# Performance work log

Hardware: AMD Instinct MI355X
Metric: run time of the kernel (lower is better)

## Reference

```python
import jax, jax.numpy as jnp
import numpy as np

B, N, M, C = 4, 4096, 300, 1152
SA_H, SA_D = 36, 32           # linear self-attention heads / head dim
CA_H = 16                     # cross-attention heads
INNER_SA = SA_H * SA_D        # 1152
INNER_FF = int(C * 2.5)       # 2880
EPS = 1e-6


def _ln(x):
    # LayerNorm without affine, eps=1e-6
    mu = x.mean(-1, keepdims=True)
    var = x.var(-1, keepdims=True)
    return (x - mu) / jnp.sqrt(var + EPS)


def setup_inputs() -> dict:
    key = jax.random.key(0)
    ks = jax.random.split(key, 24)
    p = lambda i, shape: jax.random.normal(ks[i], shape, jnp.float32) * 0.02
    return {
        "x": jax.random.normal(ks[0], (B, N, C), jnp.float32),
        "conditioning": jax.random.normal(ks[1], (B, M, C), jnp.float32),
        "t_emb": jax.random.normal(ks[2], (B, C), jnp.float32),
        # linear self-attention (qkv has no bias)
        "w_qkv": p(3, (C, 3 * INNER_SA)),
        "w_sa_out": p(4, (INNER_SA, C)),
        "b_sa_out": jnp.zeros((C,), jnp.float32),
        # norm_cross (affine LayerNorm)
        "gamma_cross": jnp.ones((C,), jnp.float32),
        "beta_cross": jnp.zeros((C,), jnp.float32),
        # cross-attention
        "w_q": p(5, (C, C)), "b_q": jnp.zeros((C,), jnp.float32),
        "w_kv": p(6, (C, 2 * C)), "b_kv": jnp.zeros((2 * C,), jnp.float32),
        "w_co": p(7, (C, C)), "b_co": jnp.zeros((C,), jnp.float32),
        # MixFFN
        "w_fc1": p(8, (C, 2 * INNER_FF)), "b_fc1": jnp.zeros((2 * INNER_FF,), jnp.float32),
        "dw_kernel": p(9, (3, 3, 1, INNER_FF)),  # depthwise conv, HWIO
        "dw_bias": jnp.zeros((INNER_FF,), jnp.float32),
        "w_fc2": p(10, (INNER_FF, C)), "b_fc2": jnp.zeros((C,), jnp.float32),
        # adaLN modulation
        "w_ada": p(11, (C, 6 * C)), "b_ada": jnp.zeros((6 * C,), jnp.float32),
        "sst": jax.random.normal(ks[12], (6, C), jnp.float32) * 0.02,
    }


def reference(x, conditioning, t_emb, w_qkv, w_sa_out, b_sa_out,
              gamma_cross, beta_cross, w_q, b_q, w_kv, b_kv, w_co, b_co,
              w_fc1, b_fc1, dw_kernel, dw_bias, w_fc2, b_fc2,
              w_ada, b_ada, sst):
    Bx, Nx, Cx = x.shape
    ada = jax.nn.silu(t_emb) @ w_ada + b_ada          # (B, 6C)
    ada = sst[None] + ada.reshape(Bx, 6, Cx)          # (B, 6, C)
    shift_sa, scale_sa, gate_sa, shift_ff, scale_ff, gate_ff = (
        ada[:, 0], ada[:, 1], ada[:, 2], ada[:, 3], ada[:, 4], ada[:, 5])

    # --- modulated linear self-attention (ReLU kernel) ---
    xn = _ln(x) * (1.0 + scale_sa[:, None]) + shift_sa[:, None]
    qkv = (xn @ w_qkv).reshape(Bx, Nx, 3, SA_H, SA_D)
    q = jax.nn.relu(qkv[:, :, 0])
    k = jax.nn.relu(qkv[:, :, 1])
    v = qkv[:, :, 2]
    kv = jnp.einsum('bnhd,bnhe->bhde', k, v)                  # (B,H,D,D)
    out = jnp.einsum('bnhd,bhde->bnhe', q, kv)                # (B,N,H,D)
    denom = jnp.einsum('bnhd,bhd->bnh', q, k.sum(1)) + 1e-6   # (B,N,H)
    out = (out / denom[..., None]).reshape(Bx, Nx, INNER_SA)
    x = x + gate_sa[:, None] * (out @ w_sa_out + b_sa_out)

    # --- cross-attention (softmax) ---
    xc = _ln(x) * gamma_cross + beta_cross
    hd = Cx // CA_H
    qc = (xc @ w_q + b_q).reshape(Bx, Nx, CA_H, hd)
    kvc = (conditioning @ w_kv + b_kv).reshape(Bx, M, 2, CA_H, hd)
    kc, vc = kvc[:, :, 0], kvc[:, :, 1]
    attn = jnp.einsum('bnhd,bmhd->bhnm', qc, kc) * (hd ** -0.5)
    attn = jax.nn.softmax(attn, axis=-1)
    oc = jnp.einsum('bhnm,bmhd->bnhd', attn, vc).reshape(Bx, Nx, Cx)
    x = x + oc @ w_co + b_co

    # --- modulated GLU-dwconv FFN ---
    xn = _ln(x) * (1.0 + scale_ff[:, None]) + shift_ff[:, None]
    gv = xn @ w_fc1 + b_fc1
    gate, val = gv[..., :INNER_FF], gv[..., INNER_FF:]
    h = jax.nn.silu(gate) * val
    hw = int(round(Nx ** 0.5))
    h = h.reshape(Bx, hw, hw, INNER_FF)                       # NHWC
    h = jax.lax.conv_general_dilated(
        h, dw_kernel, window_strides=(1, 1), padding='SAME',
        dimension_numbers=('NHWC', 'HWIO', 'NHWC'),
        feature_group_count=INNER_FF) + dw_bias
    h = h.reshape(Bx, Nx, INNER_FF)
    x = x + gate_ff[:, None] * (h @ w_fc2 + b_fc2)
    return x
```

## Files before the change

kernel.cpp:

```cpp
#include <hip/hip_runtime.h>

typedef __bf16 bf16_t;
typedef __attribute__((ext_vector_type(8))) __bf16 bf16x8;
typedef __attribute__((ext_vector_type(4))) __bf16 bf16x4;
typedef __attribute__((ext_vector_type(4))) float f32x4;

#define DEVINL __device__ __forceinline__

DEVINL void gload16(const void* g, void* l) {
  __builtin_amdgcn_global_load_lds(
      (const __attribute__((address_space(1))) void*)g,
      (__attribute__((address_space(3))) void*)l, 16, 0, 0);
}

template <int OUT>
__global__ __launch_bounds__(512) void gemm256r(
    const bf16_t* __restrict__ A, const bf16_t* __restrict__ Bt,
    void* __restrict__ Cv, int M, int N, int K,
    const float* __restrict__ bias, const float* __restrict__ resid,
    const float* __restrict__ gate, int GM)
{
  __shared__ __align__(16) bf16_t sL[4][2][256 * 32];
  const int tid = threadIdx.x;
  const int lane = tid & 63;
  const int wave = tid >> 6;
  const int wr = wave >> 2;
  const int wc = wave & 3;

  const int nbx = gridDim.x, nby = gridDim.y;
  const int nwg = nbx * nby;
  int lin = (int)blockIdx.y * nbx + (int)blockIdx.x;
  {
    const int q = nwg >> 3, rr = nwg & 7;
    const int xcd = lin & 7, idx = lin >> 3;
    lin = (xcd < rr ? xcd * (q + 1) : rr * (q + 1) + (xcd - rr) * q) + idx;
  }
  const int per_grp = GM * nbx;
  const int gid = lin / per_grp;
  const int rem = lin - gid * per_grp;
  const int gsz = min(GM, nby - gid * GM);
  const long tileM = (long)(gid * GM + rem % gsz) * 256;
  const long tileN = (long)(rem / gsz) * 256;

  const int r0 = tid >> 2;
  const int c0 = (((tid & 3) - (r0 >> 2)) & 3) * 8;

  auto STAGE = [&](int slot, int kt) {
    const bf16_t* ga = A + (tileM + r0) * (long)K + kt + c0;
    const bf16_t* gb = Bt + (tileN + r0) * (long)K + kt + c0;
    char* la = (char*)&sL[slot][0][0] + tid * 16;
    char* lb = (char*)&sL[slot][1][0] + tid * 16;
    gload16(ga, la);
    gload16(ga + 128 * (long)K, la + 8192);
    gload16(gb, lb);
    gload16(gb + 128 * (long)K, lb + 8192);
  };

  f32x4 acc[8][4] = {};
  const int NT = K >> 5;

  STAGE(0, 0); STAGE(1, 32); STAGE(2, 64);
  asm volatile("s_waitcnt vmcnt(8)" ::: "memory");
  asm volatile("s_barrier" ::: "memory");

  const int r = lane & 15;
  const int kg = lane >> 4;
  const int sw = ((kg + (r >> 2)) & 3) * 16;
  const int abyte = (wr * 128 + r) * 64 + sw;
  const int bbyte = (wc * 64 + r) * 64 + sw;

  for (int t = 0; t < NT; ++t) {
    if (t + 3 < NT) STAGE((t + 3) & 3, (t + 3) << 5);
    const char* pA = (const char*)&sL[t & 3][0][0];
    const char* pB = (const char*)&sL[t & 3][1][0];
    bf16x8 a[8], b[4];
#pragma unroll
    for (int n = 0; n < 4; ++n) b[n] = *(const bf16x8*)(pB + bbyte + n * 1024);
#pragma unroll
    for (int m = 0; m < 8; ++m) a[m] = *(const bf16x8*)(pA + abyte + m * 1024);
    __builtin_amdgcn_s_setprio(1);
#pragma unroll
    for (int m = 0; m < 8; ++m)
#pragma unroll
      for (int n = 0; n < 4; ++n)
        acc[m][n] = __builtin_amdgcn_mfma_f32_16x16x32_bf16(a[m], b[n],
                                                            acc[m][n], 0, 0, 0);
    __builtin_amdgcn_s_setprio(0);
    if (t + 1 >= NT) break;
    if (t + 3 < NT)       asm volatile("s_waitcnt vmcnt(8)" ::: "memory");
    else if (t + 3 == NT) asm volatile("s_waitcnt vmcnt(4)" ::: "memory");
    else                  asm volatile("s_waitcnt vmcnt(0)" ::: "memory");
    asm volatile("s_barrier" ::: "memory");
  }

  const long row0 = tileM + wr * 128 + ((lane >> 4) * 4);
  const int col0 = (int)tileN + wc * 64 + r;
  if constexpr (OUT == 4) {
#pragma unroll
    for (int m = 0; m < 8; ++m) {
#pragma unroll
      for (int n = 0; n < 4; n += 2) {
        const int base = (int)tileN + wc * 64 + n * 16;
        if (base < 5760) {
          const int hcol = (base >> 1) + r;
          const float bg = bias[hcol];
          const float bv = bias[2880 + hcol];
#pragma unroll
          for (int j = 0; j < 4; ++j) {
            const long row = row0 + m * 16 + j;
            const float g = acc[m][n][j] + bg;
            const float v = acc[m][n + 1][j] + bv;
            const float sg = g / (1.0f + __expf(-g));
            ((bf16_t*)Cv)[row * 2880 + hcol] = (bf16_t)(sg * v);
          }
        }
      }
    }
    return;
  }
#pragma unroll
  for (int m = 0; m < 8; ++m) {
#pragma unroll
    for (int n = 0; n < 4; ++n) {
      const int col = col0 + n * 16;
      if (col < N) {
        const float bb = bias ? bias[col] : 0.0f;
#pragma unroll
        for (int j = 0; j < 4; ++j) {
          const long row = row0 + m * 16 + j;
          const long idx = row * (long)N + col;
          const float v = acc[m][n][j] + bb;
          if constexpr (OUT == 1) {
            const float g = gate ? gate[(row >> 12) * 6912 + col] : 1.0f;
            const float rv = resid ? resid[idx] : 0.0f;
            ((float*)Cv)[idx] = rv + g * v;
          } else {
            ((bf16_t*)Cv)[idx] = (bf16_t)v;
          }
        }
      }
    }
  }
}

template <int OUT>
__global__ __launch_bounds__(256) void gemm_bt(
    const bf16_t* __restrict__ A, const bf16_t* __restrict__ Bt,
    void* __restrict__ Cv, int M, int N, int K,
    long strideA, long strideB, long strideC,
    const float* __restrict__ bias, const float* __restrict__ resid,
    const float* __restrict__ gate, int GM)
{
  __shared__ __align__(16) bf16_t sA[128 * 32];
  __shared__ __align__(16) bf16_t sB[128 * 32];
  const int tid = threadIdx.x;
  const int lane = tid & 63;
  const int wave = tid >> 6;
  const bf16_t* Ab = A + (size_t)blockIdx.z * strideA;
  const bf16_t* Bb = Bt + (size_t)blockIdx.z * strideB;

  const int nbx = gridDim.x, nby = gridDim.y;
  const int nwg = nbx * nby;
  int lin = (int)blockIdx.y * nbx + (int)blockIdx.x;
  {
    const int q = nwg >> 3, rr = nwg & 7;
    const int xcd = lin & 7, idx = lin >> 3;
    lin = (xcd < rr ? xcd * (q + 1) : rr * (q + 1) + (xcd - rr) * q) + idx;
  }
  const int per_grp = GM * nbx;
  const int gid = lin / per_grp;
  const int rem = lin - gid * per_grp;
  const int gsz = min(GM, nby - gid * GM);
  const long tileM = (long)(gid * GM + rem % gsz) * 128;
  const long tileN = (long)(rem / gsz) * 128;
  const int wr = wave >> 1, wc = wave & 1;

  f32x4 acc[4][4] = {};

  const int srow = lane >> 2;
  const int skcol = (lane & 3) * 8;
  const bf16_t* gA0 = Ab + (tileM + wave * 16 + srow) * (long)K + skcol;
  const bf16_t* gB0 = Bb + (tileN + wave * 16 + srow) * (long)K + skcol;
  bf16_t* lA0 = sA + wave * 512;
  bf16_t* lB0 = sB + wave * 512;
  const long rs64 = 64L * K;

  const int aoff = (wr * 64 + (lane & 15)) * 32 + (lane >> 4) * 8;
  const int boff = (wc * 64 + (lane & 15)) * 32 + (lane >> 4) * 8;

  for (int kt = 0; kt < K; kt += 32) {
    __syncthreads();
    gload16(gA0 + kt, lA0);
    gload16(gA0 + kt + rs64, lA0 + 2048);
    gload16(gB0 + kt, lB0);
    gload16(gB0 + kt + rs64, lB0 + 2048);
    __syncthreads();
    bf16x8 av[4], bv[4];
#pragma unroll
    for (int m = 0; m < 4; ++m) av[m] = *(const bf16x8*)&sA[aoff + m * 512];
#pragma unroll
    for (int n = 0; n < 4; ++n) bv[n] = *(const bf16x8*)&sB[boff + n * 512];
#pragma unroll
    for (int m = 0; m < 4; ++m)
#pragma unroll
      for (int n = 0; n < 4; ++n)
        acc[m][n] = __builtin_amdgcn_mfma_f32_16x16x32_bf16(av[m], bv[n],
                                                            acc[m][n], 0, 0, 0);
  }

  const long row0 = tileM + wr * 64 + ((lane >> 4) * 4);
  const int col0 = (int)tileN + wc * 64 + (lane & 15);
#pragma unroll
  for (int m = 0; m < 4; ++m) {
#pragma unroll
    for (int n = 0; n < 4; ++n) {
      const int col = col0 + n * 16;
      const float bb = (OUT != 2 && bias) ? bias[col] : 0.0f;
#pragma unroll
      for (int j = 0; j < 4; ++j) {
        const long row = row0 + m * 16 + j;
        const float v = acc[m][n][j] + bb;
        if constexpr (OUT == 1) {
          const long idx = row * (long)N + col;
          const float g = gate ? gate[(row >> 12) * 6912 + col] : 1.0f;
          const float rv = resid ? resid[idx] : 0.0f;
          ((float*)Cv)[idx] = rv + g * v;
        } else if constexpr (OUT == 2) {
          if (col < 72)
            ((bf16_t*)Cv)[(((long)(blockIdx.z >> 4)) * 4096 + row) * 1152 +
                          (long)(blockIdx.z & 15) * 72 + col] = (bf16_t)v;
        } else if constexpr (OUT == 3) {
          const int h = col / 72, d = col - h * 72;
          const long b = row >> 12, n4 = row & 4095;
          ((bf16_t*)Cv)[((b * 16 + h) * 4096 + n4) * 96 + d] =
              (bf16_t)(v * 0.11785113019775793f);
        } else {
          const long idx = row * (long)N + col;
          (((bf16_t*)Cv) + (size_t)blockIdx.z * strideC)[idx] = (bf16_t)v;
        }
      }
    }
  }
}

__global__ __launch_bounds__(256) void transpose_cast(
    const float* __restrict__ W, bf16_t* __restrict__ WT, int K, int N)
{
  __shared__ float tile[32][33];
  const int n0 = blockIdx.x * 32, k0 = blockIdx.y * 32;
  const int tx = threadIdx.x & 31, ty = threadIdx.x >> 5;
#pragma unroll
  for (int r = ty; r < 32; r += 8) tile[r][tx] = W[(size_t)(k0 + r) * N + n0 + tx];
  __syncthreads();
#pragma unroll
  for (int r = ty; r < 32; r += 8)
    WT[(size_t)(n0 + r) * K + k0 + tx] = (bf16_t)tile[tx][r];
}

__global__ __launch_bounds__(256) void transpose_glu(
    const float* __restrict__ W, bf16_t* __restrict__ WT)
{
  __shared__ float tile[32][33];
  const int b = blockIdx.x;
  const int k0 = blockIdx.y * 32;
  const int tx = threadIdx.x & 31, ty = threadIdx.x >> 5;
  if (b < 180) {
    const int src = (tx < 16) ? (b * 16 + tx) : (2880 + b * 16 + tx - 16);
#pragma unroll
    for (int r = ty; r < 32; r += 8)
      tile[r][tx] = W[(size_t)(k0 + r) * 5760 + src];
  }
  __syncthreads();
#pragma unroll
  for (int o = ty; o < 32; o += 8)
    WT[(size_t)(b * 32 + o) * 1152 + k0 + tx] =
        (b < 180) ? (bf16_t)tile[tx][o] : (bf16_t)0.0f;
}

__global__ __launch_bounds__(256) void ada_kernel(
    const float* __restrict__ t_emb, const float* __restrict__ w_ada,
    const float* __restrict__ b_ada, const float* __restrict__ sst,
    float* __restrict__ ada)
{
  __shared__ float st[4][1152];
  const int t = threadIdx.x;
  const int j = blockIdx.x * 256 + t;
  for (int i = t; i < 4 * 1152; i += 256) {
    const int b = i / 1152, cc = i % 1152;
    const float v = t_emb[b * 1152 + cc];
    st[b][cc] = v / (1.0f + __expf(-v));
  }
  __syncthreads();
  const int k0 = blockIdx.y * 144;
  float a0 = 0.f, a1 = 0.f, a2 = 0.f, a3 = 0.f;
  for (int k = k0; k < k0 + 144; ++k) {
    const float w = w_ada[(size_t)k * 6912 + j];
    a0 += st[0][k] * w; a1 += st[1][k] * w;
    a2 += st[2][k] * w; a3 += st[3][k] * w;
  }
  if (blockIdx.y == 0) {
    const float base = b_ada[j] + sst[j];
    a0 += base; a1 += base; a2 += base; a3 += base;
  }
  atomicAdd(&ada[0 * 6912 + j], a0);
  atomicAdd(&ada[1 * 6912 + j], a1);
  atomicAdd(&ada[2 * 6912 + j], a2);
  atomicAdd(&ada[3 * 6912 + j], a3);
}

__global__ __launch_bounds__(256) void ln_mod(
    const float* __restrict__ X, bf16_t* __restrict__ out,
    const float* __restrict__ adaB, int shiftIdx, int scaleIdx,
    const float* __restrict__ gamma, const float* __restrict__ beta)
{
  const int row = blockIdx.x;
  const float4* xr4 = (const float4*)(X + (size_t)row * 1152);
  float s = 0.f, s2 = 0.f;
  for (int i = threadIdx.x; i < 288; i += 256) {
    const float4 v = xr4[i];
    s += v.x + v.y + v.z + v.w;
    s2 += v.x * v.x + v.y * v.y + v.z * v.z + v.w * v.w;
  }
  const int lane = threadIdx.x & 63, wave = threadIdx.x >> 6;
#pragma unroll
  for (int o = 32; o; o >>= 1) { s += __shfl_down(s, o); s2 += __shfl_down(s2, o); }
  __shared__ float rs[4], rq[4];
  if (lane == 0) { rs[wave] = s; rq[wave] = s2; }
  __syncthreads();
  if (threadIdx.x == 0) {
    rs[0] = rs[0] + rs[1] + rs[2] + rs[3];
    rq[0] = rq[0] + rq[1] + rq[2] + rq[3];
  }
  __syncthreads();
  const float mu = rs[0] * (1.0f / 1152.0f);
  const float var = rq[0] * (1.0f / 1152.0f) - mu * mu;
  const float inv = rsqrtf(var + 1e-6f);
  const int b = row >> 12;
  const float4* shiftv = (const float4*)(adaB ? adaB + b * 6912 + shiftIdx * 1152 : beta);
  const float4* scalev = (const float4*)(adaB ? adaB + b * 6912 + scaleIdx * 1152 : gamma);
  const float add1 = adaB ? 1.0f : 0.0f;
  for (int i = threadIdx.x; i < 288; i += 256) {
    const float4 v = xr4[i];
    const float4 sc = scalev[i];
    const float4 sh = shiftv[i];
    bf16x4 o;
    o[0] = (bf16_t)((v.x - mu) * inv * (add1 + sc.x) + sh.x);
    o[1] = (bf16_t)((v.y - mu) * inv * (add1 + sc.y) + sh.y);
    o[2] = (bf16_t)((v.z - mu) * inv * (add1 + sc.z) + sh.z);
    o[3] = (bf16_t)((v.w - mu) * inv * (add1 + sc.w) + sh.w);
    *(bf16x4*)&out[(size_t)row * 1152 + i * 4] = o;
  }
}

__global__ void pad_cond_k(const float* __restrict__ cond, bf16_t* __restrict__ condp)
{
  const int idx = blockIdx.x * 256 + threadIdx.x;
  const int row = idx / 1152;
  condp[idx] = (row < 1200) ? (bf16_t)cond[idx] : (bf16_t)0.0f;
}

__global__ __launch_bounds__(256) void sa_kv_k(
    const bf16_t* __restrict__ qkv, float* __restrict__ kvb, float* __restrict__ ksumb)
{
  const int bh = blockIdx.x, b = bh / 36, h = bh % 36;
  __shared__ bf16_t sk[32][32], sv[32][32];
  const int t = threadIdx.x;
  const int nn = t >> 5, c = t & 31;
  const int srow = (t & 127) >> 2;
  const int sq4 = (t & 3) * 8;
  const int isV = t >> 7;
  float a0 = 0.f, a1 = 0.f, a2 = 0.f, a3 = 0.f, ks = 0.f;
  const size_t rowbase = (size_t)b * 4096 + (size_t)blockIdx.y * 256;
  const size_t colbase = 1152 + (size_t)isV * 1152 + h * 32 + sq4;
  for (int n0 = 0; n0 < 256; n0 += 32) {
    __syncthreads();
    const bf16x8 v8 = *(const bf16x8*)&qkv[(rowbase + n0 + srow) * 3456 + colbase];
    if (isV == 0) {
      bf16x8 r8;
#pragma unroll
      for (int j = 0; j < 8; ++j) r8[j] = (bf16_t)fmaxf((float)v8[j], 0.0f);
      *(bf16x8*)&sk[srow][sq4] = r8;
    } else {
      *(bf16x8*)&sv[srow][sq4] = v8;
    }
    __syncthreads();
#pragma unroll
    for (int q = 0; q < 32; ++q) {
      const float vv = (float)sv[q][c];
      a0 += (float)sk[q][nn] * vv;
      a1 += (float)sk[q][nn + 8] * vv;
      a2 += (float)sk[q][nn + 16] * vv;
      a3 += (float)sk[q][nn + 24] * vv;
    }
    if (t < 32) {
#pragma unroll
      for (int q = 0; q < 32; ++q) ks += (float)sk[q][t];
    }
  }
  float* kvp = kvb + (size_t)bh * 1024;
  atomicAdd(&kvp[(nn + 0) * 32 + c], a0);
  atomicAdd(&kvp[(nn + 8) * 32 + c], a1);
  atomicAdd(&kvp[(nn + 16) * 32 + c], a2);
  atomicAdd(&kvp[(nn + 24) * 32 + c], a3);
  if (t < 32) atomicAdd(&ksumb[bh * 32 + t], ks);
}

__global__ __launch_bounds__(256) void sa_out_k(
    const bf16_t* __restrict__ qkv, const float* __restrict__ kvb,
    const float* __restrict__ ksumb, bf16_t* __restrict__ so)
{
  const int row0 = blockIdx.x * 8;
  const int b = row0 >> 12;
  __shared__ float q[8][1152];
  __shared__ float denom[8][36];
  const int t = threadIdx.x;
  for (int i = t; i < 1152; i += 256) {
    const int r = i / 144, c0 = (i % 144) * 8;
    const bf16x8 v8 = *(const bf16x8*)&qkv[(size_t)(row0 + r) * 3456 + c0];
#pragma unroll
    for (int j = 0; j < 8; ++j) q[r][c0 + j] = fmaxf((float)v8[j], 0.0f);
  }
  __syncthreads();
  for (int i = t; i < 288; i += 256) {
    int r = i / 36, h = i % 36;
    const float* ksp = ksumb + (b * 36 + h) * 32;
    float dsum = 1e-6f;
#pragma unroll
    for (int d = 0; d < 32; ++d) dsum += q[r][h * 32 + d] * ksp[d];
    denom[r][h] = dsum;
  }
  __syncthreads();
  for (int j = t; j < 1152; j += 256) {
    const int h = j >> 5, e = j & 31;
    const float* kvp = kvb + ((size_t)(b * 36 + h)) * 1024 + e;
    float kreg[32];
#pragma unroll
    for (int d = 0; d < 32; ++d) kreg[d] = kvp[d * 32];
#pragma unroll
    for (int r = 0; r < 8; ++r) {
      float a = 0.f;
#pragma unroll
      for (int d = 0; d < 32; ++d) a += q[r][h * 32 + d] * kreg[d];
      so[(size_t)(row0 + r) * 1152 + j] = (bf16_t)(a / denom[r][h]);
    }
  }
}

__global__ void ca_qrepack(const bf16_t* __restrict__ qc, bf16_t* __restrict__ qcp, int b)
{
  const size_t idx = (size_t)blockIdx.x * 256 + threadIdx.x;
  const int d = (int)(idx % 96);
  const size_t r = idx / 96;
  const int n = (int)(r & 4095);
  const int h = (int)(r >> 12);
  float v = 0.f;
  if (d < 72) v = (float)qc[((size_t)(b * 4096 + n)) * 1152 + h * 72 + d] * 0.11785113019775793f;
  qcp[idx] = (bf16_t)v;
}

__global__ void ca_kcrepack(const bf16_t* __restrict__ kvc, bf16_t* __restrict__ kcp, int b)
{
  const size_t idx = (size_t)blockIdx.x * 256 + threadIdx.x;
  const int d = (int)(idx % 96);
  const size_t r = idx / 96;
  const int m = (int)(r % 384);
  const int h = (int)(r / 384);
  bf16_t v = (bf16_t)0.0f;
  if (d < 72 && m < 300) v = kvc[((size_t)(b * 300 + m)) * 2304 + h * 72 + d];
  kcp[idx] = v;
}

__global__ void ca_vtrepack(const bf16_t* __restrict__ kvc, bf16_t* __restrict__ vt, int b)
{
  const size_t idx = (size_t)blockIdx.x * 256 + threadIdx.x;
  const int m = (int)(idx % 384);
  const size_t r = idx / 384;
  const int d = (int)(r & 127);
  const int h = (int)(r >> 7);
  bf16_t v = (bf16_t)0.0f;
  if (d < 72 && m < 300) v = kvc[((size_t)(b * 300 + m)) * 2304 + 1152 + h * 72 + d];
  vt[idx] = v;
}

__global__ __launch_bounds__(256) void softmax_k(bf16_t* __restrict__ s)
{
  const int row = blockIdx.x * 4 + (threadIdx.x >> 6);
  const int lane = threadIdx.x & 63;
  bf16_t* sr = s + (size_t)row * 384;
  float v[5];
  float mx = -1e30f;
#pragma unroll
  for (int i = 0; i < 5; ++i) {
    const int m = lane + 64 * i;
    v[i] = (m < 300) ? (float)sr[m] : -1e30f;
    mx = fmaxf(mx, v[i]);
  }
#pragma unroll
  for (int o = 32; o; o >>= 1) mx = fmaxf(mx, __shfl_xor(mx, o));
  float sum = 0.f;
#pragma unroll
  for (int i = 0; i < 5; ++i) { v[i] = __expf(v[i] - mx); sum += v[i]; }
#pragma unroll
  for (int o = 32; o; o >>= 1) sum += __shfl_xor(sum, o);
  const float inv = 1.0f / sum;
#pragma unroll
  for (int i = 0; i < 5; ++i) {
    const int m = lane + 64 * i;
    if (m < 320) sr[m] = (bf16_t)(v[i] * inv);
  }
}

__global__ __launch_bounds__(256) void dwconv_k(
    const bf16_t* __restrict__ h, const float* __restrict__ wk,
    const float* __restrict__ wb, bf16_t* __restrict__ hc)
{
  const size_t idx = (size_t)blockIdx.x * 256 + threadIdx.x;
  const int c8 = (int)(idx % 360);
  size_t p = idx / 360;
  const int x = (int)(p & 63);
  const int y = (int)((p >> 6) & 63);
  const int b = (int)(p >> 12);
  const int c0 = c8 * 8;
  float acc[8];
#pragma unroll
  for (int j = 0; j < 8; ++j) acc[j] = wb[c0 + j];
  for (int ky = -1; ky <= 1; ++ky) {
    const int yy = y + ky;
    if (yy < 0 || yy > 63) continue;
    for (int kx = -1; kx <= 1; ++kx) {
      const int xx = x + kx;
      if (xx < 0 || xx > 63) continue;
      const bf16x8 v = *(const bf16x8*)&h[((size_t)(b * 4096 + yy * 64 + xx)) * 2880 + c0];
      const float* w = wk + ((ky + 1) * 3 + (kx + 1)) * 2880 + c0;
#pragma unroll
      for (int j = 0; j < 8; ++j) acc[j] += (float)v[j] * w[j];
    }
  }
  bf16x8 o;
#pragma unroll
  for (int j = 0; j < 8; ++j) o[j] = (bf16_t)acc[j];
  *(bf16x8*)&hc[((size_t)(b * 4096 + y * 64 + x)) * 2880 + c0] = o;
}

extern "C" void kernel_launch(void* const* d_in, const int* in_sizes, int n_in,
                              void* d_out, int out_size, void* d_ws, size_t ws_size,
                              hipStream_t stream)
{
  const float* x          = (const float*)d_in[0];
  const float* cond       = (const float*)d_in[1];
  const float* t_emb      = (const float*)d_in[2];
  const float* w_qkv      = (const float*)d_in[3];
  const float* w_sa_out   = (const float*)d_in[4];
  const float* b_sa_out   = (const float*)d_in[5];
  const float* gamma_cr   = (const float*)d_in[6];
  const float* beta_cr    = (const float*)d_in[7];
  const float* w_q        = (const float*)d_in[8];
  const float* b_q        = (const float*)d_in[9];
  const float* w_kv       = (const float*)d_in[10];
  const float* b_kv       = (const float*)d_in[11];
  const float* w_co       = (const float*)d_in[12];
  const float* b_co       = (const float*)d_in[13];
  const float* w_fc1      = (const float*)d_in[14];
  const float* b_fc1      = (const float*)d_in[15];
  const float* dw_kernel  = (const float*)d_in[16];
  const float* dw_bias    = (const float*)d_in[17];
  const float* w_fc2      = (const float*)d_in[18];
  const float* b_fc2      = (const float*)d_in[19];
  const float* w_ada      = (const float*)d_in[20];
  const float* b_ada      = (const float*)d_in[21];
  const float* sst        = (const float*)d_in[22];
  float* out = (float*)d_out;

  char* ws = (char*)d_ws;
  size_t off = 0;
  auto alloc = [&](size_t bytes) -> char* {
    off = (off + 255) & ~(size_t)255;
    char* p = ws + off;
    off += bytes;
    return p;
  };

  bf16_t* wqkvT  = (bf16_t*)alloc((size_t)3584 * 1152 * 2);
  bf16_t* wsaT   = (bf16_t*)alloc((size_t)1280 * 1152 * 2);
  bf16_t* wqT    = (bf16_t*)alloc((size_t)1280 * 1152 * 2);
  bf16_t* wkvT   = (bf16_t*)alloc((size_t)2304 * 1152 * 2);
  bf16_t* wcoT   = (bf16_t*)alloc((size_t)1280 * 1152 * 2);
  bf16_t* wfc1P  = (bf16_t*)alloc((size_t)5888 * 1152 * 2);
  bf16_t* wfc2T  = (bf16_t*)alloc((size_t)1280 * 2880 * 2);
  float*  adaB   = (float*)alloc((size_t)4 * 6912 * 4);
  bf16_t* xn     = (bf16_t*)alloc((size_t)16384 * 1152 * 2);
  bf16_t* buf37  = (bf16_t*)alloc((size_t)16384 * 1152 * 2);
  float*  kvb    = (float*)alloc((size_t)144 * 1024 * 4);
  float*  ksumb  = (float*)alloc((size_t)144 * 32 * 4);
  bf16_t* condp  = (bf16_t*)alloc((size_t)1280 * 1152 * 2);
  bf16_t* kvcB   = (bf16_t*)alloc((size_t)1280 * 2304 * 2);

  const size_t ARENA_SMALL = (size_t)16384 * 3456 * 2;
  const size_t CA_Q = (size_t)64 * 4096 * 96 * 2;
  const size_t CA_K = (size_t)64 * 384 * 96 * 2;
  const size_t CA_V = (size_t)64 * 128 * 384 * 2;
  const size_t CA_S = (size_t)64 * 4096 * 384 * 2;
  const size_t ARENA_BIG = CA_Q + CA_K + CA_V + CA_S;
  const bool big = (off + 512 + ARENA_BIG) <= ws_size;
  char* arena = alloc(big ? ARENA_BIG : ARENA_SMALL);
  if (off > ws_size) return;

  bf16_t* qkvB = (bf16_t*)arena;
  bf16_t *qcp, *kcp, *vcT, *scores;
  if (big) {
    qcp    = (bf16_t*)arena;
    kcp    = (bf16_t*)(arena + CA_Q);
    vcT    = (bf16_t*)(arena + CA_Q + CA_K);
    scores = (bf16_t*)(arena + CA_Q + CA_K + CA_V);
  } else {
    qcp    = (bf16_t*)arena;
    kcp    = (bf16_t*)(arena + 12582912);
    vcT    = (bf16_t*)(arena + 12582912 + 1179648);
    scores = (bf16_t*)(arena + 12582912 + 1179648 + 1572864);
  }
  bf16_t *hB, *hcB;
  if (big) {
    hB  = (bf16_t*)arena;
    hcB = (bf16_t*)(arena + (size_t)16384 * 2880 * 2);
  } else {
    hcB = (bf16_t*)arena;
    hB  = buf37;
  }

  hipMemsetAsync(adaB, 0, (size_t)4 * 6912 * 4, stream);
  hipMemsetAsync(kvb, 0, (size_t)144 * 1024 * 4, stream);
  hipMemsetAsync(ksumb, 0, (size_t)144 * 32 * 4, stream);

  transpose_cast<<<dim3(108, 36), 256, 0, stream>>>(w_qkv, wqkvT, 1152, 3456);
  transpose_cast<<<dim3(36, 36), 256, 0, stream>>>(w_sa_out, wsaT, 1152, 1152);
  transpose_cast<<<dim3(36, 36), 256, 0, stream>>>(w_q, wqT, 1152, 1152);
  transpose_cast<<<dim3(72, 36), 256, 0, stream>>>(w_kv, wkvT, 1152, 2304);
  transpose_cast<<<dim3(36, 36), 256, 0, stream>>>(w_co, wcoT, 1152, 1152);
  transpose_glu<<<dim3(184, 36), 256, 0, stream>>>(w_fc1, wfc1P);
  transpose_cast<<<dim3(36, 90), 256, 0, stream>>>(w_fc2, wfc2T, 2880, 1152);
  ada_kernel<<<dim3(27, 8), 256, 0, stream>>>(t_emb, w_ada, b_ada, sst, adaB);
  pad_cond_k<<<5760, 256, 0, stream>>>(cond, condp);

  ln_mod<<<16384, 256, 0, stream>>>(x, xn, adaB, 0, 1, nullptr, nullptr);
  gemm256r<0><<<dim3(14, 64), 512, 0, stream>>>(xn, wqkvT, qkvB, 16384, 3456, 1152,
                                                nullptr, nullptr, nullptr, 8);
  sa_kv_k<<<dim3(144, 16), 256, 0, stream>>>(qkvB, kvb, ksumb);
  sa_out_k<<<2048, 256, 0, stream>>>(qkvB, kvb, ksumb, buf37);
  gemm_bt<1><<<dim3(9, 128), 256, 0, stream>>>(buf37, wsaT, out, 16384, 1152, 1152,
                                               0, 0, 0, b_sa_out, x, adaB + 2 * 1152, 8);

  ln_mod<<<16384, 256, 0, stream>>>(out, xn, nullptr, 0, 0, gamma_cr, beta_cr);
  gemm_bt<0><<<dim3(18, 10, 1), 256, 0, stream>>>(condp, wkvT, kvcB, 1280, 2304, 1152,
                                                  0, 0, 0, b_kv, nullptr, nullptr, 8);
  if (big) {
    hipMemsetAsync(qcp, 0, CA_Q, stream);
    gemm_bt<3><<<dim3(9, 128), 256, 0, stream>>>(xn, wqT, qcp, 16384, 1152, 1152,
                                                 0, 0, 0, b_q, nullptr, nullptr, 8);
    for (int b = 0; b < 4; ++b) {
      ca_kcrepack<<<2304, 256, 0, stream>>>(kvcB, kcp + (size_t)b * 16 * 384 * 96, b);
      ca_vtrepack<<<3072, 256, 0, stream>>>(kvcB, vcT + (size_t)b * 16 * 128 * 384, b);
    }
    gemm_bt<0><<<dim3(3, 32, 64), 256, 0, stream>>>(qcp, kcp, scores, 4096, 384, 96,
                                                    (long)4096 * 96, (long)384 * 96,
                                                    (long)4096 * 384, nullptr, nullptr, nullptr, 8);
    softmax_k<<<65536, 256, 0, stream>>>(scores);
    gemm_bt<2><<<dim3(1, 32, 64), 256, 0, stream>>>(scores, vcT, buf37, 4096, 128, 384,
                                                    (long)4096 * 384, (long)128 * 384,
                                                    0, nullptr, nullptr, nullptr, 8);
  } else {
    gemm_bt<0><<<dim3(9, 128), 256, 0, stream>>>(xn, wqT, buf37, 16384, 1152, 1152,
                                                 0, 0, 0, b_q, nullptr, nullptr, 8);
    for (int b = 0; b < 4; ++b) {
      ca_qrepack<<<24576, 256, 0, stream>>>(buf37, qcp, b);
      ca_kcrepack<<<2304, 256, 0, stream>>>(kvcB, kcp, b);
      ca_vtrepack<<<3072, 256, 0, stream>>>(kvcB, vcT, b);
      gemm_bt<0><<<dim3(3, 32, 16), 256, 0, stream>>>(qcp, kcp, scores, 4096, 384, 96,
                                                      (long)4096 * 96, (long)384 * 96,
                                                      (long)4096 * 384, nullptr, nullptr, nullptr, 8);
      softmax_k<<<16384, 256, 0, stream>>>(scores);
      gemm_bt<2><<<dim3(1, 32, 16), 256, 0, stream>>>(scores, vcT,
                                                      buf37 + (size_t)b * 4096 * 1152,
                                                      4096, 128, 384,
                                                      (long)4096 * 384, (long)128 * 384,
                                                      0, nullptr, nullptr, nullptr, 8);
    }
  }
  gemm_bt<1><<<dim3(9, 128), 256, 0, stream>>>(buf37, wcoT, out, 16384, 1152, 1152,
                                               0, 0, 0, b_co, out, nullptr, 8);

  ln_mod<<<16384, 256, 0, stream>>>(out, xn, adaB, 3, 4, nullptr, nullptr);
  if (big) {
    gemm256r<4><<<dim3(23, 64), 512, 0, stream>>>(xn, wfc1P, hB, 16384, 5760, 1152,
                                                  b_fc1, nullptr, nullptr, 8);
    dwconv_k<<<23040, 256, 0, stream>>>(hB, dw_kernel, dw_bias, hcB);
    gemm_bt<1><<<dim3(9, 128), 256, 0, stream>>>(hcB, wfc2T, out, 16384, 1152, 2880,
                                                 0, 0, 0, b_fc2, out,
                                                 adaB + 5 * 1152, 8);
  } else {
    for (int c = 0; c < 2; ++c) {
      for (int bb = 0; bb < 2; ++bb) {
        const int b = c * 2 + bb;
        gemm256r<4><<<dim3(23, 16), 512, 0, stream>>>(xn + (size_t)b * 4096 * 1152, wfc1P,
                                                      hB, 4096, 5760, 1152,
                                                      b_fc1, nullptr, nullptr, 8);
        dwconv_k<<<5760, 256, 0, stream>>>(hB, dw_kernel, dw_bias,
                                           hcB + (size_t)bb * 4096 * 2880);
      }
      gemm_bt<1><<<dim3(9, 64), 256, 0, stream>>>(hcB, wfc2T,
                                                  out + (size_t)c * 8192 * 1152,
                                                  8192, 1152, 2880, 0, 0, 0, b_fc2,
                                                  out + (size_t)c * 8192 * 1152,
                                                  adaB + (size_t)c * 2 * 6912 + 5 * 1152, 8);
    }
  }

  (void)in_sizes; (void)n_in; (void)out_size; (void)ws_size;
}
```

Measured before the change: 1.790 ms.

## Fuse cross-attention score GEMM with softmax; use 3-stage LDS ring in gemm256r

```diff
diff --git a/kernel.cpp b/kernel.cpp
--- a/kernel.cpp
+++ b/kernel.cpp
@@ -20,7 +20,7 @@
     const float* __restrict__ bias, const float* __restrict__ resid,
     const float* __restrict__ gate, int GM)
 {
-  __shared__ __align__(16) bf16_t sL[4][2][256 * 32];
+  __shared__ __align__(16) bf16_t sL[3][2][256 * 32];
   const int tid = threadIdx.x;
   const int lane = tid & 63;
   const int wave = tid >> 6;
@@ -69,10 +69,10 @@
   const int abyte = (wr * 128 + r) * 64 + sw;
   const int bbyte = (wc * 64 + r) * 64 + sw;
 
+  int slot = 0;
   for (int t = 0; t < NT; ++t) {
-    if (t + 3 < NT) STAGE((t + 3) & 3, (t + 3) << 5);
-    const char* pA = (const char*)&sL[t & 3][0][0];
-    const char* pB = (const char*)&sL[t & 3][1][0];
+    const char* pA = (const char*)&sL[slot][0][0];
+    const char* pB = (const char*)&sL[slot][1][0];
     bf16x8 a[8], b[4];
 #pragma unroll
     for (int n = 0; n < 4; ++n) b[n] = *(const bf16x8*)(pB + bbyte + n * 1024);
@@ -87,10 +87,11 @@
                                                             acc[m][n], 0, 0, 0);
     __builtin_amdgcn_s_setprio(0);
     if (t + 1 >= NT) break;
-    if (t + 3 < NT)       asm volatile("s_waitcnt vmcnt(8)" ::: "memory");
-    else if (t + 3 == NT) asm volatile("s_waitcnt vmcnt(4)" ::: "memory");
-    else                  asm volatile("s_waitcnt vmcnt(0)" ::: "memory");
+    if (t + 2 < NT) asm volatile("s_waitcnt vmcnt(4)" ::: "memory");
+    else            asm volatile("s_waitcnt vmcnt(0)" ::: "memory");
     asm volatile("s_barrier" ::: "memory");
+    if (t + 3 < NT) STAGE(slot, (t + 3) << 5);
+    slot = (slot == 2) ? 0 : slot + 1;
   }
 
   const long row0 = tileM + wr * 128 + ((lane >> 4) * 4);
@@ -238,6 +239,106 @@
           const long idx = row * (long)N + col;
           (((bf16_t*)Cv) + (size_t)blockIdx.z * strideC)[idx] = (bf16_t)v;
         }
+      }
+    }
+  }
+}
+
+__global__ __launch_bounds__(256) void ca_scores_sm(
+    const bf16_t* __restrict__ qcp, const bf16_t* __restrict__ kcp,
+    bf16_t* __restrict__ P)
+{
+  __shared__ __align__(16) bf16_t sA[128 * 32];
+  __shared__ __align__(16) bf16_t sB[384 * 32];
+  __shared__ float smax[128][2];
+  __shared__ float ssum[128][2];
+  const int tid = threadIdx.x;
+  const int lane = tid & 63;
+  const int wave = tid >> 6;
+  const int wr = wave >> 1, wc = wave & 1;
+  const int bh = blockIdx.y;
+  const long m0 = (long)blockIdx.x * 128;
+  const bf16_t* Qb = qcp + (size_t)bh * 4096 * 96;
+  const bf16_t* Kb = kcp + (size_t)bh * 384 * 96;
+
+  f32x4 acc[4][12] = {};
+  const int l15 = lane & 15, g = lane >> 4;
+  const int aoff = (wr * 64 + l15) * 32 + g * 8;
+
+  for (int kt = 0; kt < 96; kt += 32) {
+    __syncthreads();
+#pragma unroll
+    for (int r2 = 0; r2 < 2; ++r2) {
+      const int c = tid + r2 * 256;
+      gload16(Qb + (m0 + (c >> 2)) * 96 + kt + (c & 3) * 8, (char*)sA + c * 16);
+    }
+#pragma unroll
+    for (int r2 = 0; r2 < 6; ++r2) {
+      const int c = tid + r2 * 256;
+      gload16(Kb + (size_t)(c >> 2) * 96 + kt + (c & 3) * 8, (char*)sB + c * 16);
+    }
+    asm volatile("s_waitcnt vmcnt(0)" ::: "memory");
+    __syncthreads();
+    bf16x8 a[4];
+#pragma unroll
+    for (int mf = 0; mf < 4; ++mf) a[mf] = *(const bf16x8*)&sA[aoff + mf * 512];
+#pragma unroll
+    for (int nf = 0; nf < 12; ++nf) {
+      const bf16x8 b = *(const bf16x8*)&sB[(wc * 192 + nf * 16 + l15) * 32 + g * 8];
+#pragma unroll
+      for (int mf = 0; mf < 4; ++mf)
+        acc[mf][nf] = __builtin_amdgcn_mfma_f32_16x16x32_bf16(a[mf], b,
+                                                              acc[mf][nf], 0, 0, 0);
+    }
+  }
+
+#pragma unroll
+  for (int mf = 0; mf < 4; ++mf) {
+#pragma unroll
+    for (int j = 0; j < 4; ++j) {
+      float mx = -1e30f;
+#pragma unroll
+      for (int nf = 0; nf < 12; ++nf) {
+        const int col = wc * 192 + nf * 16 + l15;
+        if (col < 300) mx = fmaxf(mx, acc[mf][nf][j]);
+      }
+#pragma unroll
+      for (int o = 1; o < 16; o <<= 1) mx = fmaxf(mx, __shfl_xor(mx, o));
+      if (l15 == 0) smax[wr * 64 + mf * 16 + g * 4 + j][wc] = mx;
+    }
+  }
+  __syncthreads();
+#pragma unroll
+  for (int mf = 0; mf < 4; ++mf) {
+#pragma unroll
+    for (int j = 0; j < 4; ++j) {
+      const int row = wr * 64 + mf * 16 + g * 4 + j;
+      const float gm = fmaxf(smax[row][0], smax[row][1]);
+      float s = 0.f;
+#pragma unroll
+      for (int nf = 0; nf < 12; ++nf) {
+        const int col = wc * 192 + nf * 16 + l15;
+        const float e = (col < 300) ? __expf(acc[mf][nf][j] - gm) : 0.0f;
+        acc[mf][nf][j] = e;
+        s += e;
+      }
+#pragma unroll
+      for (int o = 1; o < 16; o <<= 1) s += __shfl_xor(s, o);
+      if (l15 == 0) ssum[row][wc] = s;
+    }
+  }
+  __syncthreads();
+#pragma unroll
+  for (int mf = 0; mf < 4; ++mf) {
+#pragma unroll
+    for (int j = 0; j < 4; ++j) {
+      const int row = wr * 64 + mf * 16 + g * 4 + j;
+      const float inv = 1.0f / (ssum[row][0] + ssum[row][1]);
+#pragma unroll
+      for (int nf = 0; nf < 12; ++nf) {
+        const int col = wc * 192 + nf * 16 + l15;
+        P[((size_t)bh * 4096 + m0 + row) * 384 + col] =
+            (bf16_t)(acc[mf][nf][j] * inv);
       }
     }
   }
@@ -653,17 +754,13 @@
   gemm_bt<0><<<dim3(18, 10, 1), 256, 0, stream>>>(condp, wkvT, kvcB, 1280, 2304, 1152,
                                                   0, 0, 0, b_kv, nullptr, nullptr, 8);
   if (big) {
-    hipMemsetAsync(qcp, 0, CA_Q, stream);
     gemm_bt<3><<<dim3(9, 128), 256, 0, stream>>>(xn, wqT, qcp, 16384, 1152, 1152,
                                                  0, 0, 0, b_q, nullptr, nullptr, 8);
     for (int b = 0; b < 4; ++b) {
       ca_kcrepack<<<2304, 256, 0, stream>>>(kvcB, kcp + (size_t)b * 16 * 384 * 96, b);
       ca_vtrepack<<<3072, 256, 0, stream>>>(kvcB, vcT + (size_t)b * 16 * 128 * 384, b);
     }
-    gemm_bt<0><<<dim3(3, 32, 64), 256, 0, stream>>>(qcp, kcp, scores, 4096, 384, 96,
-                                                    (long)4096 * 96, (long)384 * 96,
-                                                    (long)4096 * 384, nullptr, nullptr, nullptr, 8);
-    softmax_k<<<65536, 256, 0, stream>>>(scores);
+    ca_scores_sm<<<dim3(32, 64), 256, 0, stream>>>(qcp, kcp, scores);
     gemm_bt<2><<<dim3(1, 32, 64), 256, 0, stream>>>(scores, vcT, buf37, 4096, 128, 384,
                                                     (long)4096 * 384, (long)128 * 384,
                                                     0, nullptr, nullptr, nullptr, 8);
```

Measured after the change: 1.790 ms, median of 2. About the same (-0.0%).
